# Kernel tuning notes

Measured on AMD Instinct MI355X. Metric: run time of the kernel, lower is better.

## Reference

```python
import jax, jax.numpy as jnp
import numpy as np

IN_FEATURES = 2048
OUT_FEATURES = 8192
HARMONICS = 256
TWO_PI = 2.0 * np.pi


def setup_inputs() -> dict:
    key = jax.random.key(0)
    kx, kb, kp = jax.random.split(key, 3)
    x = jax.random.normal(kx, (4, 4096, IN_FEATURES), dtype=jnp.float32)
    # basis: randn then L2-normalized along in_features (dim=1), as in torch buffer init
    basis = jax.random.normal(kb, (HARMONICS, IN_FEATURES), dtype=jnp.float32)
    basis = basis / jnp.linalg.norm(basis, axis=1, keepdims=True)
    phase = jax.random.normal(kp, (OUT_FEATURES, HARMONICS), dtype=jnp.float32) * TWO_PI
    amp = jnp.ones((OUT_FEATURES, HARMONICS), dtype=jnp.float32) / HARMONICS
    return {"x": x, "basis": basis, "phase": phase, "amp": amp}


def reference(x, basis, phase, amp):
    # resonance = x @ basis.T : [..., harmonics]
    resonance = jnp.einsum("bsi,hi->bsh", x, basis)
    # Real part of (resonance + 0i) * (amp*cos(phase) + i*amp*sin(phase)) summed over h
    # collapses to resonance @ (amp * cos(phase)).T -- identical math, no complex dtype.
    w_real = amp * jnp.cos(phase)  # [out, harmonics]
    return jnp.einsum("bsh,oh->bso", resonance, w_real)
```

## Files before the change

### kernel.cpp

```cpp
#include <hip/hip_runtime.h>
#include <hip/hip_bf16.h>
#include <stdint.h>
#include <stddef.h>


typedef __bf16 bf16x8 __attribute__((ext_vector_type(8)));
typedef float  f32x4  __attribute__((ext_vector_type(4)));
typedef float  f32x16 __attribute__((ext_vector_type(16)));
typedef unsigned short u16x8 __attribute__((ext_vector_type(8)));

#define M_ROWS 16384
#define K_IN   2048
#define N_OUT  8192
#define N_HARM 256

__device__ inline unsigned short f2bf(float f) {
    union { float f; uint32_t u; } c; c.f = f;
    uint32_t u = c.u;
    uint32_t r = (u + 0x7fffu + ((u >> 16) & 1u)) >> 16;
    return (unsigned short)r;
}

__device__ inline bf16x8 cvt8(f32x4 a, f32x4 b) {
    bf16x8 r;
    r[0] = (__bf16)a[0]; r[1] = (__bf16)a[1]; r[2] = (__bf16)a[2]; r[3] = (__bf16)a[3];
    r[4] = (__bf16)b[0]; r[5] = (__bf16)b[1]; r[6] = (__bf16)b[2]; r[7] = (__bf16)b[3];
    return r;
}

#define GLDS(src, dst) \
    __builtin_amdgcn_global_load_lds((const __attribute__((address_space(1))) void*)(src), \
                                     (__attribute__((address_space(3))) void*)(dst), 16, 0, 0)

__global__ __launch_bounds__(256) void cvt_bf16(const float* __restrict__ in,
                                                unsigned short* __restrict__ out) {
    size_t i = ((size_t)blockIdx.x * 256 + threadIdx.x) * 8;
    f32x4 v0 = *(const f32x4*)(in + i);
    f32x4 v1 = *(const f32x4*)(in + i + 4);
    u16x8 o;
    o[0] = f2bf(v0[0]); o[1] = f2bf(v0[1]); o[2] = f2bf(v0[2]); o[3] = f2bf(v0[3]);
    o[4] = f2bf(v1[0]); o[5] = f2bf(v1[1]); o[6] = f2bf(v1[2]); o[7] = f2bf(v1[3]);
    *(u16x8*)(out + i) = o;
}

__global__ __launch_bounds__(256) void wreal_bf16(const float* __restrict__ phase,
                                                  const float* __restrict__ amp,
                                                  unsigned short* __restrict__ out) {
    size_t i = ((size_t)blockIdx.x * 256 + threadIdx.x) * 8;
    f32x4 p0 = *(const f32x4*)(phase + i);
    f32x4 p1 = *(const f32x4*)(phase + i + 4);
    f32x4 a0 = *(const f32x4*)(amp + i);
    f32x4 a1 = *(const f32x4*)(amp + i + 4);
    u16x8 o;
    o[0] = f2bf(a0[0] * cosf(p0[0])); o[1] = f2bf(a0[1] * cosf(p0[1]));
    o[2] = f2bf(a0[2] * cosf(p0[2])); o[3] = f2bf(a0[3] * cosf(p0[3]));
    o[4] = f2bf(a1[0] * cosf(p1[0])); o[5] = f2bf(a1[1] * cosf(p1[1]));
    o[6] = f2bf(a1[2] * cosf(p1[2])); o[7] = f2bf(a1[3] * cosf(p1[3]));
    *(u16x8*)(out + i) = o;
}

__global__ __launch_bounds__(256) void gemm1_fused(const float* __restrict__ A,
                                                   const unsigned short* __restrict__ B,
                                                   unsigned short* __restrict__ C) {
    __shared__ float          Asm[2][32 * 64];
    __shared__ unsigned short Bsm[2][256 * 64];

    const int tid  = threadIdx.x;
    const int lane = tid & 63;
    const int wv   = tid >> 6;
    const int bm0  = blockIdx.x * 32;

    const float* srcA[2];
#pragma unroll
    for (int q = 0; q < 2; ++q) {
        int L = q * 256 + tid;
        int r = L >> 4, p = L & 15;
        int c = p ^ (r & 15);
        srcA[q] = A + (size_t)(bm0 + r) * K_IN + c * 4;
    }
    const unsigned short* srcB[8];
#pragma unroll
    for (int q = 0; q < 8; ++q) {
        int L = q * 256 + tid;
        int r = L >> 3, p = L & 7;
        int c = p ^ (r & 7);
        srcB[q] = B + (size_t)r * K_IN + c * 8;
    }
    const int dA = wv * 256 + lane * 4;
    const int dB = wv * 512 + lane * 8;

    f32x16 acc[2];
#pragma unroll
    for (int nf = 0; nf < 2; ++nf)
#pragma unroll
        for (int e = 0; e < 16; ++e) acc[nf][e] = 0.f;

    const int r   = lane & 31;
    const int g   = lane >> 5;
    const int r15 = r & 15;
    const int colb = wv * 64;

#pragma unroll
    for (int q = 0; q < 2; ++q) GLDS(srcA[q], &Asm[0][q * 1024 + dA]);
#pragma unroll
    for (int q = 0; q < 8; ++q) GLDS(srcB[q], &Bsm[0][q * 2048 + dB]);
    __syncthreads();

    for (int t = 0; t < 32; ++t) {
        const int buf = t & 1;
        if (t + 1 < 32) {
            const int k0 = (t + 1) * 64;
#pragma unroll
            for (int q = 0; q < 2; ++q) GLDS(srcA[q] + k0, &Asm[buf ^ 1][q * 1024 + dA]);
#pragma unroll
            for (int q = 0; q < 8; ++q) GLDS(srcB[q] + k0, &Bsm[buf ^ 1][q * 2048 + dB]);
        }

        bf16x8 af[4];
#pragma unroll
        for (int ks = 0; ks < 4; ++ks) {
            const int c0 = g * 2 + ks * 4;
            f32x4 lo = *(const f32x4*)&Asm[buf][r * 64 + ((c0)     ^ r15) * 4];
            f32x4 hi = *(const f32x4*)&Asm[buf][r * 64 + ((c0 + 1) ^ r15) * 4];
            af[ks] = cvt8(lo, hi);
        }
#pragma unroll
        for (int nf = 0; nf < 2; ++nf) {
            const int rB = colb + nf * 32 + r;
            const int r7 = rB & 7;
#pragma unroll
            for (int ks = 0; ks < 4; ++ks) {
                const int cB = g + ks * 2;
                bf16x8 bfrag = *(const bf16x8*)&Bsm[buf][rB * 64 + (cB ^ r7) * 8];
                acc[nf] = __builtin_amdgcn_mfma_f32_32x32x16_bf16(af[ks], bfrag, acc[nf], 0, 0, 0);
            }
        }
        __syncthreads();
    }

#pragma unroll
    for (int nf = 0; nf < 2; ++nf)
#pragma unroll
        for (int reg = 0; reg < 16; ++reg) {
            int row = bm0 + (reg & 3) + 8 * (reg >> 2) + 4 * g;
            int col = colb + nf * 32 + r;
            C[(size_t)row * N_HARM + col] = f2bf(acc[nf][reg]);
        }
}

__global__ __launch_bounds__(512) void gemm2_nstream(const unsigned short* __restrict__ A,
                                                     const unsigned short* __restrict__ B,
                                                     float* __restrict__ Cv) {
    __shared__ unsigned short As[3][32 * 256];

    const int tid  = threadIdx.x;
    const int lane = tid & 63;
    const int wv   = tid >> 6;
    const int r    = lane & 31;
    const int g    = lane >> 5;
    const int r7   = r & 7;

    const int col0  = blockIdx.x * 256 + wv * 32;
    const int mbase = blockIdx.y * 1024;

    bf16x8 bf[16];
#pragma unroll
    for (int ks = 0; ks < 16; ++ks)
        bf[ks] = *(const bf16x8*)(B + (size_t)(col0 + r) * N_HARM + ks * 16 + g * 8);

    const unsigned short* srcA[2];
#pragma unroll
    for (int q = 0; q < 2; ++q) {
        int L = q * 512 + tid;
        int row = L >> 5, slot = L & 31;
        int c = slot ^ (row & 7);
        srcA[q] = A + (size_t)(mbase + row) * N_HARM + c * 8;
    }
    const int dstA = tid * 8;

    GLDS(srcA[0], &As[0][dstA]);
    GLDS(srcA[1], &As[0][4096 + dstA]);
    __syncthreads();

    for (int t = 0; t < 32; ++t) {
        const int cur = t % 3;
        if (t + 1 < 32) {
            const int nxt = (t + 1) % 3;
            __builtin_amdgcn_sched_barrier(0);
            GLDS(srcA[0] + (t + 1) * 32 * N_HARM, &As[nxt][dstA]);
            GLDS(srcA[1] + (t + 1) * 32 * N_HARM, &As[nxt][4096 + dstA]);
            __builtin_amdgcn_sched_barrier(0);
        }

        f32x16 acc;
#pragma unroll
        for (int e = 0; e < 16; ++e) acc[e] = 0.f;

#pragma unroll
        for (int ks = 0; ks < 16; ++ks) {
            const int c = ks * 2 + g;
            bf16x8 af = *(const bf16x8*)&As[cur][r * 256 + (c ^ r7) * 8];
            acc = __builtin_amdgcn_mfma_f32_32x32x16_bf16(af, bf[ks], acc, 0, 0, 0);
        }

        const int m0 = mbase + t * 32;
#pragma unroll
        for (int reg = 0; reg < 16; ++reg) {
            int row = m0 + (reg & 3) + 8 * (reg >> 2) + 4 * g;
            Cv[(size_t)row * N_OUT + col0 + r] = acc[reg];
        }

        __syncthreads();
    }
}

extern "C" void kernel_launch(void* const* d_in, const int* in_sizes, int n_in,
                              void* d_out, int out_size, void* d_ws, size_t ws_size,
                              hipStream_t stream) {
    const float* x     = (const float*)d_in[0];
    const float* basis = (const float*)d_in[1];
    const float* phase = (const float*)d_in[2];
    const float* amp   = (const float*)d_in[3];
    float* out = (float*)d_out;

    char* ws = (char*)d_ws;
    unsigned short* bb  = (unsigned short*)(ws);
    unsigned short* wrb = (unsigned short*)(ws + 1048576);
    unsigned short* rb  = (unsigned short*)(ws + 5242880);

    cvt_bf16<<<dim3(256), dim3(256), 0, stream>>>(basis, bb);
    wreal_bf16<<<dim3(1024), dim3(256), 0, stream>>>(phase, amp, wrb);

    gemm1_fused<<<dim3(M_ROWS / 32), dim3(256), 0, stream>>>(x, bb, rb);
    gemm2_nstream<<<dim3(32, 16), dim3(512), 0, stream>>>(rb, wrb, out);
}
```

Measured before the change: 188.5 us.

## Keep a 256-row A tile resident in LDS for the second GEMM

The second GEMM no longer streams A through a triple-buffered LDS ring. Each block now loads a full 256x256 bf16 A tile (128KB) into LDS once, then sweeps eight 256-column panels of W, reloading the B fragments into registers per panel. The grid shrinks from 512 to 256 blocks. This removes the repeated A traffic and per-step barriers, but adds an unoverlapped upfront load, per-panel B register reloads with no prefetch, and allows only one block per CU, which leaves fewer waves to keep the large fp32 output stores flowing.

```diff
diff --git a/kernel.cpp b/kernel.cpp
--- a/kernel.cpp
+++ b/kernel.cpp
@@ -148,10 +148,10 @@
         }
 }
 
-__global__ __launch_bounds__(512) void gemm2_nstream(const unsigned short* __restrict__ A,
-                                                     const unsigned short* __restrict__ B,
-                                                     float* __restrict__ Cv) {
-    __shared__ unsigned short As[3][32 * 256];
+__global__ __launch_bounds__(512) void gemm2_astat(const unsigned short* __restrict__ A,
+                                                   const unsigned short* __restrict__ B,
+                                                   float* __restrict__ Cv) {
+    __shared__ unsigned short As[256 * 256];
 
     const int tid  = threadIdx.x;
     const int lane = tid & 63;
@@ -160,57 +160,49 @@
     const int g    = lane >> 5;
     const int r7   = r & 7;
 
-    const int col0  = blockIdx.x * 256 + wv * 32;
-    const int mbase = blockIdx.y * 1024;
-
-    bf16x8 bf[16];
-#pragma unroll
-    for (int ks = 0; ks < 16; ++ks)
-        bf[ks] = *(const bf16x8*)(B + (size_t)(col0 + r) * N_HARM + ks * 16 + g * 8);
-
-    const unsigned short* srcA[2];
-#pragma unroll
-    for (int q = 0; q < 2; ++q) {
-        int L = q * 512 + tid;
-        int row = L >> 5, slot = L & 31;
-        int c = slot ^ (row & 7);
-        srcA[q] = A + (size_t)(mbase + row) * N_HARM + c * 8;
-    }
-    const int dstA = tid * 8;
-
-    GLDS(srcA[0], &As[0][dstA]);
-    GLDS(srcA[1], &As[0][4096 + dstA]);
+    const int mbase = (blockIdx.x >> 2) * 256;
+    const int nbase = (blockIdx.x & 3) * 2048;
+
+    {
+        const int trow = tid >> 5;
+        const int slot = tid & 31;
+        const int c    = slot ^ (trow & 7);
+        const unsigned short* src = A + (size_t)(mbase + trow) * N_HARM + c * 8;
+        const int dst = tid * 8;
+#pragma unroll
+        for (int q = 0; q < 16; ++q)
+            GLDS(src + (size_t)q * 16 * N_HARM, &As[q * 4096 + dst]);
+    }
     __syncthreads();
 
-    for (int t = 0; t < 32; ++t) {
-        const int cur = t % 3;
-        if (t + 1 < 32) {
-            const int nxt = (t + 1) % 3;
-            __builtin_amdgcn_sched_barrier(0);
-            GLDS(srcA[0] + (t + 1) * 32 * N_HARM, &As[nxt][dstA]);
-            GLDS(srcA[1] + (t + 1) * 32 * N_HARM, &As[nxt][4096 + dstA]);
-            __builtin_amdgcn_sched_barrier(0);
-        }
-
-        f32x16 acc;
-#pragma unroll
-        for (int e = 0; e < 16; ++e) acc[e] = 0.f;
-
-#pragma unroll
-        for (int ks = 0; ks < 16; ++ks) {
-            const int c = ks * 2 + g;
-            bf16x8 af = *(const bf16x8*)&As[cur][r * 256 + (c ^ r7) * 8];
-            acc = __builtin_amdgcn_mfma_f32_32x32x16_bf16(af, bf[ks], acc, 0, 0, 0);
-        }
-
-        const int m0 = mbase + t * 32;
-#pragma unroll
-        for (int reg = 0; reg < 16; ++reg) {
-            int row = m0 + (reg & 3) + 8 * (reg >> 2) + 4 * g;
-            Cv[(size_t)row * N_OUT + col0 + r] = acc[reg];
-        }
-
-        __syncthreads();
+    for (int panel = 0; panel < 8; ++panel) {
+        const int col0 = nbase + panel * 256 + wv * 32;
+
+        bf16x8 bf[16];
+#pragma unroll
+        for (int ks = 0; ks < 16; ++ks)
+            bf[ks] = *(const bf16x8*)(B + (size_t)(col0 + r) * N_HARM + ks * 16 + g * 8);
+
+#pragma unroll
+        for (int chunk = 0; chunk < 8; ++chunk) {
+            f32x16 acc;
+#pragma unroll
+            for (int e = 0; e < 16; ++e) acc[e] = 0.f;
+
+#pragma unroll
+            for (int ks = 0; ks < 16; ++ks) {
+                const int c = ks * 2 + g;
+                bf16x8 af = *(const bf16x8*)&As[(chunk * 32 + r) * 256 + (c ^ r7) * 8];
+                acc = __builtin_amdgcn_mfma_f32_32x32x16_bf16(af, bf[ks], acc, 0, 0, 0);
+            }
+
+            const int m0 = mbase + chunk * 32;
+#pragma unroll
+            for (int reg = 0; reg < 16; ++reg) {
+                int row = m0 + (reg & 3) + 8 * (reg >> 2) + 4 * g;
+                Cv[(size_t)row * N_OUT + col0 + r] = acc[reg];
+            }
+        }
     }
 }
 
@@ -232,5 +224,5 @@
     wreal_bf16<<<dim3(1024), dim3(256), 0, stream>>>(phase, amp, wrb);
 
     gemm1_fused<<<dim3(M_ROWS / 32), dim3(256), 0, stream>>>(x, bb, rb);
-    gemm2_nstream<<<dim3(32, 16), dim3(512), 0, stream>>>(rb, wrb, out);
-}
+    gemm2_astat<<<dim3(256), dim3(512), 0, stream>>>(rb, wrb, out);
+}
```

Measured after the change: 214.9 us. 1.14x slower.
